# Kernel optimization log

Measured on AMD Instinct MI355X. Metric: run time of the kernel, lower is better.

Reference implementation:

```python
import jax, jax.numpy as jnp
import numpy as np
import math

B, S, KV, D, H = 4, 512, 4096, 1024, 16
HD = D // H  # head_dim = 64


def setup_inputs() -> dict:
    key = jax.random.key(0)
    ks = jax.random.split(key, 12)
    scale = 0.02
    return {
        "x": jax.random.normal(ks[0], (B, S, D), dtype=jnp.float32),
        "xa": jax.random.normal(ks[1], (B, KV, D), dtype=jnp.float32),
        "Wq": jax.random.normal(ks[2], (D, D), dtype=jnp.float32) * scale,
        "bq": jax.random.normal(ks[3], (D,), dtype=jnp.float32) * scale,
        "Wk": jax.random.normal(ks[4], (D, D), dtype=jnp.float32) * scale,  # key has no bias
        "Wv": jax.random.normal(ks[5], (D, D), dtype=jnp.float32) * scale,
        "bv": jax.random.normal(ks[6], (D,), dtype=jnp.float32) * scale,
        "Wo": jax.random.normal(ks[7], (D, D), dtype=jnp.float32) * scale,
        "bo": jax.random.normal(ks[8], (D,), dtype=jnp.float32) * scale,
        "cache_k": jnp.zeros((B, H, KV, HD), dtype=jnp.float32),
        "cache_v": jnp.zeros((B, H, KV, HD), dtype=jnp.float32),
    }


def reference(x, xa, Wq, bq, Wk, Wv, bv, Wo, bo, cache_k, cache_v):
    bsz, seq_len, _ = x.shape
    kv_len = xa.shape[1]
    # projections (torch nn.Linear convention: y = x @ W^T + b)
    q = (x @ Wq.T + bq).reshape(bsz, seq_len, H, HD).transpose(0, 2, 1, 3)   # [B,H,S,HD]
    k = (xa @ Wk.T).reshape(bsz, kv_len, H, HD).transpose(0, 2, 1, 3)        # [B,H,KV,HD]
    v = (xa @ Wv.T + bv).reshape(bsz, kv_len, H, HD).transpose(0, 2, 1, 3)   # [B,H,KV,HD]
    # prefill path: scatter k/v into positions [0, kv_len) of the cache
    updated_k = cache_k.at[:, :, :kv_len, :].set(k)
    updated_v = cache_v.at[:, :, :kv_len, :].set(v)
    # attention over full cache, fp32 softmax as in the original
    scores = jnp.einsum('bhqd,bhkd->bhqk', q, updated_k) / math.sqrt(HD)
    probs = jax.nn.softmax(scores.astype(jnp.float32), axis=-1).astype(q.dtype)
    attn = jnp.einsum('bhqk,bhkd->bhqd', probs, updated_v)                   # [B,H,S,HD]
    attn = attn.transpose(0, 2, 1, 3).reshape(bsz, seq_len, H * HD)
    out = attn @ Wo.T + bo
    return out, updated_k, updated_v
```

## Files before the change

kernel.cpp:

```cpp
#include <hip/hip_runtime.h>
#include <hip/hip_bf16.h>

using u16 = unsigned short;
typedef __bf16 bf16x8 __attribute__((ext_vector_type(8)));
typedef float f32x4 __attribute__((ext_vector_type(4)));

#define SB 4
#define SS 512
#define SKV 4096
#define SD 1024
#define SH 16
#define SHD 64
#define NSPLIT 4
#define NROWS 32768
#define QSCALE 0.18033688011112042f
#define DEFER_THR 6.0f

__device__ inline u16 f2bf(float f){
  __hip_bfloat16 h = __float2bfloat16(f);
  return __builtin_bit_cast(u16, h);
}
__device__ inline float bf2f(u16 u){
  return __builtin_bit_cast(float, (unsigned)u << 16);
}

__device__ inline bf16x8 ld_frag_g(const u16* p){
  uint4 v = *reinterpret_cast<const uint4*>(p);
  return __builtin_bit_cast(bf16x8, v);
}

__device__ inline bf16x8 ld_frag_lds(const char* base, int ob){
  uint4 v = *reinterpret_cast<const uint4*>(base + ob);
  return __builtin_bit_cast(bf16x8, v);
}

__device__ inline unsigned pack_bf_trunc(float a, float b){
  return __builtin_amdgcn_perm(__builtin_bit_cast(unsigned, b),
                               __builtin_bit_cast(unsigned, a), 0x07060302u);
}

__device__ inline uint4 ld_cvt8(const float* p){
  float4 f0 = *reinterpret_cast<const float4*>(p);
  float4 f1 = *reinterpret_cast<const float4*>(p + 4);
  ushort4 a, b;
  a.x = f2bf(f0.x); a.y = f2bf(f0.y); a.z = f2bf(f0.z); a.w = f2bf(f0.w);
  b.x = f2bf(f1.x); b.y = f2bf(f1.y); b.z = f2bf(f1.z); b.w = f2bf(f1.w);
  uint4 r;
  r.x = (unsigned)a.x | ((unsigned)a.y << 16);
  r.y = (unsigned)a.z | ((unsigned)a.w << 16);
  r.z = (unsigned)b.x | ((unsigned)b.y << 16);
  r.w = (unsigned)b.z | ((unsigned)b.w << 16);
  return r;
}

__global__ __launch_bounds__(256) void cast_kernel(const float* __restrict__ src,
                                                   u16* __restrict__ dst, int n4){
  int i = blockIdx.x * 256 + threadIdx.x;
  if (i < n4){
    float4 f = reinterpret_cast<const float4*>(src)[i];
    ushort4 u;
    u.x = f2bf(f.x); u.y = f2bf(f.y); u.z = f2bf(f.z); u.w = f2bf(f.w);
    reinterpret_cast<ushort4*>(dst)[i] = u;
  }
}

__global__ __launch_bounds__(256) void cast_w4(const float* __restrict__ s0,
                                               const float* __restrict__ s1,
                                               const float* __restrict__ s2,
                                               const float* __restrict__ s3,
                                               u16* __restrict__ dst){
  int which = blockIdx.x >> 10;
  int j = (blockIdx.x & 1023) * 256 + threadIdx.x;
  const float* s = which == 0 ? s0 : which == 1 ? s1 : which == 2 ? s2 : s3;
  float4 f = reinterpret_cast<const float4*>(s)[j];
  ushort4 u;
  u.x = f2bf(f.x); u.y = f2bf(f.y); u.z = f2bf(f.z); u.w = f2bf(f.w);
  reinterpret_cast<ushort4*>(dst + (long)which * 1048576L)[j] = u;
}

enum { MODE_Q = 0, MODE_K = 1, MODE_V = 2, MODE_OUT = 3 };

template<int MODE>
__global__ __launch_bounds__(256) void gemm_bt(const u16* __restrict__ A,
                                               const u16* __restrict__ W,
                                               const float* __restrict__ bias,
                                               float* __restrict__ outF,
                                               u16* __restrict__ outB)
{
  __shared__ u16 As[2][128*64];
  __shared__ u16 Bs[2][128*64];
  const int tid  = threadIdx.x;
  const int lane = tid & 63;
  const int wm   = ((tid >> 6) >> 1) * 64;
  const int wn   = ((tid >> 6) & 1) * 64;
  const long rowBase = (long)blockIdx.x * 128;
  const long colBase = (long)blockIdx.y * 128;

  f32x4 acc[4][4];
#pragma unroll
  for (int i = 0; i < 4; i++)
#pragma unroll
    for (int j = 0; j < 4; j++)
      acc[i][j] = (f32x4){0.f, 0.f, 0.f, 0.f};

  uint4 va[4], vw[4];
#pragma unroll
  for (int i = 0; i < 4; i++){
    int u = tid + i * 256;
    int r = u >> 3, c = u & 7;
    va[i] = *reinterpret_cast<const uint4*>(A + (rowBase + r) * 1024 + c * 8);
    vw[i] = *reinterpret_cast<const uint4*>(W + (colBase + r) * 1024 + c * 8);
  }
#pragma unroll
  for (int i = 0; i < 4; i++){
    int u = tid + i * 256;
    int r = u >> 3, c = u & 7;
    int ob = (r * 128 + c * 16) ^ ((r & 7) << 4);
    *reinterpret_cast<uint4*>(reinterpret_cast<char*>(As[0]) + ob) = va[i];
    *reinterpret_cast<uint4*>(reinterpret_cast<char*>(Bs[0]) + ob) = vw[i];
  }
  __syncthreads();

  int cur = 0;
  for (int kt = 0; kt < 16; ++kt){
    uint4 va2[4], vw2[4];
    if (kt < 15){
#pragma unroll
      for (int i = 0; i < 4; i++){
        int u = tid + i * 256;
        int r = u >> 3, c = u & 7;
        va2[i] = *reinterpret_cast<const uint4*>(A + (rowBase + r) * 1024 + (kt + 1) * 64 + c * 8);
        vw2[i] = *reinterpret_cast<const uint4*>(W + (colBase + r) * 1024 + (kt + 1) * 64 + c * 8);
      }
    }
    const char* ach = reinterpret_cast<const char*>(As[cur]);
    const char* bch = reinterpret_cast<const char*>(Bs[cur]);
#pragma unroll
    for (int kk = 0; kk < 2; kk++){
      bf16x8 af[4], bfr[4];
#pragma unroll
      for (int mi = 0; mi < 4; mi++){
        int row = wm + mi * 16 + (lane & 15);
        int ob = (row * 128 + kk * 64 + (lane >> 4) * 16) ^ ((row & 7) << 4);
        af[mi] = ld_frag_lds(ach, ob);
      }
#pragma unroll
      for (int ni = 0; ni < 4; ni++){
        int row = wn + ni * 16 + (lane & 15);
        int ob = (row * 128 + kk * 64 + (lane >> 4) * 16) ^ ((row & 7) << 4);
        bfr[ni] = ld_frag_lds(bch, ob);
      }
#pragma unroll
      for (int mi = 0; mi < 4; mi++)
#pragma unroll
        for (int ni = 0; ni < 4; ni++)
          acc[mi][ni] = __builtin_amdgcn_mfma_f32_16x16x32_bf16(af[mi], bfr[ni], acc[mi][ni], 0, 0, 0);
    }
    if (kt < 15){
#pragma unroll
      for (int i = 0; i < 4; i++){
        int u = tid + i * 256;
        int r = u >> 3, c = u & 7;
        int ob = (r * 128 + c * 16) ^ ((r & 7) << 4);
        *reinterpret_cast<uint4*>(reinterpret_cast<char*>(As[cur ^ 1]) + ob) = va2[i];
        *reinterpret_cast<uint4*>(reinterpret_cast<char*>(Bs[cur ^ 1]) + ob) = vw2[i];
      }
      __syncthreads();
    }
    cur ^= 1;
  }

#pragma unroll
  for (int mi = 0; mi < 4; mi++){
#pragma unroll
    for (int ni = 0; ni < 4; ni++){
      long gn = colBase + wn + ni * 16 + (lane & 15);
      float bb = bias[gn];
#pragma unroll
      for (int r = 0; r < 4; r++){
        long gm = rowBase + wm + mi * 16 + ((lane >> 4) << 2) + r;
        float val = acc[mi][ni][r] + bb;
        if (MODE == MODE_OUT){
          outF[gm * 1024 + gn] = val;
        } else {
          long b = gm >> 9, s = gm & 511;
          long h = gn >> 6, hd = gn & 63;
          outB[((b * SH + h) * SS + s) * SHD + hd] = f2bf(val * QSCALE);
        }
      }
    }
  }
}

__global__ __launch_bounds__(256) void gemm_kv(const float* __restrict__ Axa,
                                               const u16* __restrict__ Wkb,
                                               const u16* __restrict__ Wvb,
                                               const float* __restrict__ bv,
                                               float* __restrict__ outK,
                                               u16* __restrict__ outKb,
                                               float* __restrict__ outV,
                                               u16* __restrict__ outVTb)
{
  __shared__ u16 As[2][128*64];
  __shared__ u16 Bs[2][128*64];
  const int tid  = threadIdx.x;
  const int lane = tid & 63;
  const int wm   = ((tid >> 6) >> 1) * 64;
  const int wn   = ((tid >> 6) & 1) * 64;
  const int lin  = blockIdx.x;
  const int xcd  = lin & 7;
  const int role = (lin >> 3) & 1;
  const int j    = lin >> 4;
  const long rowBase = (long)(xcd * 16 + (j >> 3)) * 128;
  const long colBase = (long)(j & 7) * 128;
  const u16* W = role ? Wvb : Wkb;

  f32x4 acc[4][4];
#pragma unroll
  for (int i = 0; i < 4; i++)
#pragma unroll
    for (int jj = 0; jj < 4; jj++)
      acc[i][jj] = (f32x4){0.f, 0.f, 0.f, 0.f};

  uint4 va[4], vw[4];
#pragma unroll
  for (int i = 0; i < 4; i++){
    int u = tid + i * 256;
    int r = u >> 3, c = u & 7;
    va[i] = ld_cvt8(Axa + (rowBase + r) * 1024 + c * 8);
    vw[i] = *reinterpret_cast<const uint4*>(W + (colBase + r) * 1024 + c * 8);
  }
#pragma unroll
  for (int i = 0; i < 4; i++){
    int u = tid + i * 256;
    int r = u >> 3, c = u & 7;
    int ob = (r * 128 + c * 16) ^ ((r & 7) << 4);
    *reinterpret_cast<uint4*>(reinterpret_cast<char*>(As[0]) + ob) = va[i];
    *reinterpret_cast<uint4*>(reinterpret_cast<char*>(Bs[0]) + ob) = vw[i];
  }
  __syncthreads();

  int cur = 0;
  for (int kt = 0; kt < 16; ++kt){
    uint4 va2[4], vw2[4];
    if (kt < 15){
#pragma unroll
      for (int i = 0; i < 4; i++){
        int u = tid + i * 256;
        int r = u >> 3, c = u & 7;
        va2[i] = ld_cvt8(Axa + (rowBase + r) * 1024 + (kt + 1) * 64 + c * 8);
        vw2[i] = *reinterpret_cast<const uint4*>(W + (colBase + r) * 1024 + (kt + 1) * 64 + c * 8);
      }
    }
    const char* ach = reinterpret_cast<const char*>(As[cur]);
    const char* bch = reinterpret_cast<const char*>(Bs[cur]);
#pragma unroll
    for (int kk = 0; kk < 2; kk++){
      bf16x8 af[4], bfr[4];
#pragma unroll
      for (int mi = 0; mi < 4; mi++){
        int row = wm + mi * 16 + (lane & 15);
        int ob = (row * 128 + kk * 64 + (lane >> 4) * 16) ^ ((row & 7) << 4);
        af[mi] = ld_frag_lds(ach, ob);
      }
#pragma unroll
      for (int ni = 0; ni < 4; ni++){
        int row = wn + ni * 16 + (lane & 15);
        int ob = (row * 128 + kk * 64 + (lane >> 4) * 16) ^ ((row & 7) << 4);
        bfr[ni] = ld_frag_lds(bch, ob);
      }
#pragma unroll
      for (int mi = 0; mi < 4; mi++)
#pragma unroll
        for (int ni = 0; ni < 4; ni++)
          acc[mi][ni] = __builtin_amdgcn_mfma_f32_16x16x32_bf16(af[mi], bfr[ni], acc[mi][ni], 0, 0, 0);
    }
    if (kt < 15){
#pragma unroll
      for (int i = 0; i < 4; i++){
        int u = tid + i * 256;
        int r = u >> 3, c = u & 7;
        int ob = (r * 128 + c * 16) ^ ((r & 7) << 4);
        *reinterpret_cast<uint4*>(reinterpret_cast<char*>(As[cur ^ 1]) + ob) = va2[i];
        *reinterpret_cast<uint4*>(reinterpret_cast<char*>(Bs[cur ^ 1]) + ob) = vw2[i];
      }
      __syncthreads();
    }
    cur ^= 1;
  }

#pragma unroll
  for (int mi = 0; mi < 4; mi++){
#pragma unroll
    for (int ni = 0; ni < 4; ni++){
      long gn = colBase + wn + ni * 16 + (lane & 15);
      long h = gn >> 6, hd = gn & 63;
      if (role){
        float bb = bv[gn];
        long gmBase = rowBase + wm + mi * 16 + ((lane >> 4) << 2);
        long b = gmBase >> 12, kv = gmBase & 4095;
        long fidx = ((b * SH + h) * SKV + kv) * SHD + hd;
        ushort4 pk;
        float v0 = acc[mi][ni][0] + bb; outV[fidx          ] = v0; pk.x = f2bf(v0);
        float v1 = acc[mi][ni][1] + bb; outV[fidx +     SHD] = v1; pk.y = f2bf(v1);
        float v2 = acc[mi][ni][2] + bb; outV[fidx + 2 * SHD] = v2; pk.z = f2bf(v2);
        float v3 = acc[mi][ni][3] + bb; outV[fidx + 3 * SHD] = v3; pk.w = f2bf(v3);
        *reinterpret_cast<ushort4*>(outVTb + ((b * SH + h) * SHD + hd) * SKV + kv) = pk;
      } else {
#pragma unroll
        for (int r = 0; r < 4; r++){
          long gm = rowBase + wm + mi * 16 + ((lane >> 4) << 2) + r;
          long b = gm >> 12, kv = gm & 4095;
          long idx = ((b * SH + h) * SKV + kv) * SHD + hd;
          float val = acc[mi][ni][r];
          outK[idx] = val;
          outKb[idx] = f2bf(val);
        }
      }
    }
  }
}

__global__ __launch_bounds__(512) void attn_partial(const u16* __restrict__ qb,
                                                    const u16* __restrict__ kb,
                                                    const u16* __restrict__ vTb,
                                                    u16* __restrict__ opartB,
                                                    float* __restrict__ ml){
  __shared__ u16 Klds[2][64 * 64];
  __shared__ u16 Vlds[2][64 * 64];
  __shared__ u16 PT[8][16 * 72];
  const int tid  = threadIdx.x;
  const int lane = tid & 63;
  const int wid  = tid >> 6;
  const int c    = lane & 15;
  const int hi   = lane >> 4;
  const long bh  = blockIdx.x;
  const int  qt  = blockIdx.y;
  const int  split = blockIdx.z;

  const u16* qp = qb + (bh * SS + qt * 128 + wid * 16 + c) * SHD + hi * 8;
  const bf16x8 bq0 = ld_frag_g(qp);
  const bf16x8 bq1 = ld_frag_g(qp + 32);

  f32x4 acc[4];
#pragma unroll
  for (int i = 0; i < 4; i++) acc[i] = (f32x4){0.f, 0.f, 0.f, 0.f};
  float mrun = -INFINITY;
  f32x4 lrunv = (f32x4){0.f, 0.f, 0.f, 0.f};

  const u16* kbase = kb  + bh * SKV * SHD;
  const u16* vbase = vTb + bh * SHD * SKV;
  u16* pt = &PT[wid][0];
  const int sr  = tid >> 3;
  const int scc = tid & 7;
  const int sob = (sr * 128 + scc * 16) ^ ((sr & 7) << 4);
  const int t0 = split * 16;

  {
    uint4 kv4 = *reinterpret_cast<const uint4*>(kbase + (t0 * 64 + sr) * SHD + scc * 8);
    uint4 vv4 = *reinterpret_cast<const uint4*>(vbase + (long)sr * SKV + t0 * 64 + scc * 8);
    *reinterpret_cast<uint4*>(reinterpret_cast<char*>(Klds[0]) + sob) = kv4;
    *reinterpret_cast<uint4*>(reinterpret_cast<char*>(Vlds[0]) + sob) = vv4;
  }
  __syncthreads();

  int cur = 0;
  for (int kt = t0; kt < t0 + 16; ++kt){
    const bool hn = kt + 1 < t0 + 16;
    uint4 kn, vn;
    if (hn){
      kn = *reinterpret_cast<const uint4*>(kbase + ((kt + 1) * 64 + sr) * SHD + scc * 8);
      vn = *reinterpret_cast<const uint4*>(vbase + (long)sr * SKV + (kt + 1) * 64 + scc * 8);
    }
    const char* kch = reinterpret_cast<const char*>(Klds[cur]);
    const char* vch = reinterpret_cast<const char*>(Vlds[cur]);

    f32x4 sT[4];
#pragma unroll
    for (int ni = 0; ni < 4; ni++){
      int krow = ni * 16 + c;
      int swz = (krow & 7) << 4;
      int a0 = (krow * 128 + hi * 16) ^ swz;
      int a1 = (krow * 128 + 64 + hi * 16) ^ swz;
      f32x4 z = (f32x4){0.f, 0.f, 0.f, 0.f};
      sT[ni] = __builtin_amdgcn_mfma_f32_16x16x32_bf16(ld_frag_lds(kch, a0), bq0, z, 0, 0, 0);
      sT[ni] = __builtin_amdgcn_mfma_f32_16x16x32_bf16(ld_frag_lds(kch, a1), bq1, sT[ni], 0, 0, 0);
    }
    f32x4 mv = __builtin_elementwise_max(__builtin_elementwise_max(sT[0], sT[1]),
                                         __builtin_elementwise_max(sT[2], sT[3]));
    float t = fmaxf(fmaxf(mv[0], mv[1]), fmaxf(mv[2], mv[3]));
    if (!__all(t <= mrun + DEFER_THR)){
      float tr = fmaxf(t, __shfl_xor(t, 16));
      tr = fmaxf(tr, __shfl_xor(tr, 32));
      float mn = fmaxf(mrun, tr);
      float al = exp2f(mrun - mn);
      lrunv *= al;
#pragma unroll
      for (int ni = 0; ni < 4; ni++) acc[ni] *= al;
      mrun = mn;
    }
#pragma unroll
    for (int ni = 0; ni < 4; ni++){
      f32x4 p;
      p[0] = exp2f(sT[ni][0] - mrun); p[1] = exp2f(sT[ni][1] - mrun);
      p[2] = exp2f(sT[ni][2] - mrun); p[3] = exp2f(sT[ni][3] - mrun);
      lrunv += p;
      unsigned lo = pack_bf_trunc(p[0], p[1]);
      unsigned hp = pack_bf_trunc(p[2], p[3]);
      uint2 w; w.x = lo; w.y = hp;
      *reinterpret_cast<uint2*>(pt + c * 72 + ni * 16 + hi * 4) = w;
    }
#pragma unroll
    for (int m = 0; m < 2; m++){
      bf16x8 pfrag = __builtin_bit_cast(bf16x8,
          *reinterpret_cast<const uint4*>(pt + c * 72 + m * 32 + hi * 8));
#pragma unroll
      for (int ni = 0; ni < 4; ni++){
        int vrow = ni * 16 + c;
        int av = (vrow * 128 + m * 64 + hi * 16) ^ ((vrow & 7) << 4);
        acc[ni] = __builtin_amdgcn_mfma_f32_16x16x32_bf16(ld_frag_lds(vch, av), pfrag, acc[ni], 0, 0, 0);
      }
    }
    if (hn){
      *reinterpret_cast<uint4*>(reinterpret_cast<char*>(Klds[cur ^ 1]) + sob) = kn;
      *reinterpret_cast<uint4*>(reinterpret_cast<char*>(Vlds[cur ^ 1]) + sob) = vn;
      __syncthreads();
    }
    cur ^= 1;
  }

  float l = (lrunv[0] + lrunv[1]) + (lrunv[2] + lrunv[3]);
  l += __shfl_xor(l, 16);
  l += __shfl_xor(l, 32);
  const long row = bh * SS + (long)qt * 128 + wid * 16 + c;
  u16* ob = opartB + ((long)split * NROWS + row) * SHD;
#pragma unroll
  for (int ni = 0; ni < 4; ni++){
    ushort4 pk;
    pk.x = f2bf(acc[ni][0]); pk.y = f2bf(acc[ni][1]);
    pk.z = f2bf(acc[ni][2]); pk.w = f2bf(acc[ni][3]);
    *reinterpret_cast<ushort4*>(ob + ni * 16 + hi * 4) = pk;
  }
  if (hi == 0){
    ml[(long)split * NROWS + row] = mrun;
    ml[(long)NSPLIT * NROWS + (long)split * NROWS + row] = l;
  }
}

__global__ __launch_bounds__(256) void attn_combine(const u16* __restrict__ opartB,
                                                    const float* __restrict__ ml,
                                                    u16* __restrict__ attnb){
  long idx4 = (long)blockIdx.x * 256 + threadIdx.x;
  long row = idx4 >> 4;
  int  c   = (int)(idx4 & 15);
  float m0 = ml[row], m1 = ml[NROWS + row], m2 = ml[2L*NROWS + row], m3 = ml[3L*NROWS + row];
  float M = fmaxf(fmaxf(m0, m1), fmaxf(m2, m3));
  float w0 = exp2f(m0 - M), w1 = exp2f(m1 - M), w2 = exp2f(m2 - M), w3 = exp2f(m3 - M);
  const float* lb = ml + (long)NSPLIT * NROWS;
  float L = w0*lb[row] + w1*lb[NROWS+row] + w2*lb[2L*NROWS+row] + w3*lb[3L*NROWS+row];
  float inv = 1.f / L;
  const ushort4* op = reinterpret_cast<const ushort4*>(opartB);
  ushort4 v0 = op[(0L*NROWS + row) * 16 + c];
  ushort4 v1 = op[(1L*NROWS + row) * 16 + c];
  ushort4 v2 = op[(2L*NROWS + row) * 16 + c];
  ushort4 v3 = op[(3L*NROWS + row) * 16 + c];
  float4 val;
  val.x = (w0*bf2f(v0.x) + w1*bf2f(v1.x) + w2*bf2f(v2.x) + w3*bf2f(v3.x)) * inv;
  val.y = (w0*bf2f(v0.y) + w1*bf2f(v1.y) + w2*bf2f(v2.y) + w3*bf2f(v3.y)) * inv;
  val.z = (w0*bf2f(v0.z) + w1*bf2f(v1.z) + w2*bf2f(v2.z) + w3*bf2f(v3.z)) * inv;
  val.w = (w0*bf2f(v0.w) + w1*bf2f(v1.w) + w2*bf2f(v2.w) + w3*bf2f(v3.w)) * inv;
  long bh = row >> 9, s = row & 511;
  long b = bh >> 4, h = bh & 15;
  ushort4 u;
  u.x = f2bf(val.x); u.y = f2bf(val.y); u.z = f2bf(val.z); u.w = f2bf(val.w);
  reinterpret_cast<ushort4*>(attnb)[((b * SS + s) * SD + h * SHD) / 4 + c] = u;
}

extern "C" void kernel_launch(void* const* d_in, const int* in_sizes, int n_in,
                              void* d_out, int out_size, void* d_ws, size_t ws_size,
                              hipStream_t stream)
{
  const float* x  = (const float*)d_in[0];
  const float* xa = (const float*)d_in[1];
  const float* Wq = (const float*)d_in[2];
  const float* bq = (const float*)d_in[3];
  const float* Wk = (const float*)d_in[4];
  const float* Wv = (const float*)d_in[5];
  const float* bv = (const float*)d_in[6];
  const float* Wo = (const float*)d_in[7];
  const float* bo = (const float*)d_in[8];

  float* outO = (float*)d_out;
  float* outK = outO + (long)SB * SS * SD;
  float* outV = outK + (long)SB * SH * SKV * SHD;

  u16* ws   = (u16*)d_ws;
  u16* xb   = ws;
  u16* xab  = xb   + 2097152L;
  u16* Wqb  = xab  + 16777216L;
  u16* Wkb  = Wqb  + 1048576L;
  u16* Wvb  = Wkb  + 1048576L;
  u16* Wob  = Wvb  + 1048576L;
  u16* qbuf = Wob  + 1048576L;
  u16* kbuf = qbuf + 2097152L;
  u16* vTbuf= kbuf + 16777216L;
  u16* mlb  = vTbuf+ 16777216L;

  u16*   attnb  = xb;
  u16*   opartB = xab;
  float* ml     = (float*)mlb;

  cast_kernel<<<2048, 256, 0, stream>>>(x,  xb,  524288);
  cast_w4    <<<4096, 256, 0, stream>>>(Wq, Wk, Wv, Wo, Wqb);

  gemm_bt<MODE_Q>   <<<dim3(16, 8), 256, 0, stream>>>(xb,  Wqb, bq, nullptr, qbuf);
  gemm_kv           <<<2048,        256, 0, stream>>>(xa, Wkb, Wvb, bv,
                                                      outK, kbuf, outV, vTbuf);
  attn_partial      <<<dim3(64, 4, NSPLIT), 512, 0, stream>>>(qbuf, kbuf, vTbuf, opartB, ml);
  attn_combine      <<<2048, 256, 0, stream>>>(opartB, ml, attnb);
  gemm_bt<MODE_OUT> <<<dim3(16, 8), 256, 0, stream>>>(attnb, Wob, bo, outO, nullptr);
}
```

Measured before the change: 295.3 us.

## Merge cast kernels and fuse Q/K/V projections into a single launch

Folds the x, xa and weight casts into one cast_all kernel, which now also pre-casts xa to bf16. The K/V GEMM therefore loads bf16 instead of converting fp32 in its load path. The Q projection (128 blocks) is merged with the K and V projections into one proj_all launch, so the small Q GEMM no longer leaves most of the GPU idle on its own and there are fewer launches. In exchange, xa makes an extra fp32 read and bf16 write pass through memory. K and V blocks for the same row tile are also no longer interleaved in launch order, which may reduce L2 reuse of xa tiles.

```diff
diff --git a/kernel.cpp b/kernel.cpp
--- a/kernel.cpp
+++ b/kernel.cpp
@@ -39,53 +39,195 @@
                                __builtin_bit_cast(unsigned, a), 0x07060302u);
 }
 
-__device__ inline uint4 ld_cvt8(const float* p){
-  float4 f0 = *reinterpret_cast<const float4*>(p);
-  float4 f1 = *reinterpret_cast<const float4*>(p + 4);
-  ushort4 a, b;
-  a.x = f2bf(f0.x); a.y = f2bf(f0.y); a.z = f2bf(f0.z); a.w = f2bf(f0.w);
-  b.x = f2bf(f1.x); b.y = f2bf(f1.y); b.z = f2bf(f1.z); b.w = f2bf(f1.w);
-  uint4 r;
-  r.x = (unsigned)a.x | ((unsigned)a.y << 16);
-  r.y = (unsigned)a.z | ((unsigned)a.w << 16);
-  r.z = (unsigned)b.x | ((unsigned)b.y << 16);
-  r.w = (unsigned)b.z | ((unsigned)b.w << 16);
-  return r;
-}
-
-__global__ __launch_bounds__(256) void cast_kernel(const float* __restrict__ src,
-                                                   u16* __restrict__ dst, int n4){
-  int i = blockIdx.x * 256 + threadIdx.x;
-  if (i < n4){
-    float4 f = reinterpret_cast<const float4*>(src)[i];
-    ushort4 u;
-    u.x = f2bf(f.x); u.y = f2bf(f.y); u.z = f2bf(f.z); u.w = f2bf(f.w);
-    reinterpret_cast<ushort4*>(dst)[i] = u;
-  }
-}
-
-__global__ __launch_bounds__(256) void cast_w4(const float* __restrict__ s0,
-                                               const float* __restrict__ s1,
-                                               const float* __restrict__ s2,
-                                               const float* __restrict__ s3,
-                                               u16* __restrict__ dst){
-  int which = blockIdx.x >> 10;
-  int j = (blockIdx.x & 1023) * 256 + threadIdx.x;
-  const float* s = which == 0 ? s0 : which == 1 ? s1 : which == 2 ? s2 : s3;
+__global__ __launch_bounds__(256) void cast_all(const float* __restrict__ x,
+                                                const float* __restrict__ xa,
+                                                const float* __restrict__ Wq,
+                                                const float* __restrict__ Wk,
+                                                const float* __restrict__ Wv,
+                                                const float* __restrict__ Wo,
+                                                u16* __restrict__ xb,
+                                                u16* __restrict__ xab,
+                                                u16* __restrict__ Wqb){
+  int bid = blockIdx.x;
+  const float* s; u16* d; long j;
+  if (bid < 2048){
+    s = x;  d = xb;  j = (long)bid * 256 + threadIdx.x;
+  } else if (bid < 18432){
+    s = xa; d = xab; j = (long)(bid - 2048) * 256 + threadIdx.x;
+  } else {
+    int wb = bid - 18432;
+    int which = wb >> 10;
+    s = which == 0 ? Wq : which == 1 ? Wk : which == 2 ? Wv : Wo;
+    d = Wqb + (long)which * 1048576L;
+    j = (long)(wb & 1023) * 256 + threadIdx.x;
+  }
   float4 f = reinterpret_cast<const float4*>(s)[j];
   ushort4 u;
   u.x = f2bf(f.x); u.y = f2bf(f.y); u.z = f2bf(f.z); u.w = f2bf(f.w);
-  reinterpret_cast<ushort4*>(dst + (long)which * 1048576L)[j] = u;
+  reinterpret_cast<ushort4*>(d)[j] = u;
 }
 
 enum { MODE_Q = 0, MODE_K = 1, MODE_V = 2, MODE_OUT = 3 };
 
-template<int MODE>
-__global__ __launch_bounds__(256) void gemm_bt(const u16* __restrict__ A,
-                                               const u16* __restrict__ W,
-                                               const float* __restrict__ bias,
-                                               float* __restrict__ outF,
-                                               u16* __restrict__ outB)
+__global__ __launch_bounds__(256) void proj_all(const u16* __restrict__ xb,
+                                                const u16* __restrict__ xab,
+                                                const u16* __restrict__ Wqb,
+                                                const u16* __restrict__ Wkb,
+                                                const u16* __restrict__ Wvb,
+                                                const float* __restrict__ bq,
+                                                const float* __restrict__ bv,
+                                                u16* __restrict__ qbuf,
+                                                float* __restrict__ outK,
+                                                u16* __restrict__ kbuf,
+                                                float* __restrict__ outV,
+                                                u16* __restrict__ vTbuf)
+{
+  __shared__ u16 As[2][128*64];
+  __shared__ u16 Bs[2][128*64];
+  const int tid  = threadIdx.x;
+  const int lane = tid & 63;
+  const int wm   = ((tid >> 6) >> 1) * 64;
+  const int wn   = ((tid >> 6) & 1) * 64;
+
+  int mode;
+  const u16 *A, *W;
+  long rowBase, colBase;
+  {
+    int bid = blockIdx.x;
+    if (bid < 128){
+      mode = MODE_Q; A = xb; W = Wqb;
+      rowBase = (long)(bid >> 3) * 128;
+      colBase = (long)(bid & 7) * 128;
+    } else {
+      int lin = bid - 128;
+      if (lin < 1024){ mode = MODE_K; W = Wkb; }
+      else           { mode = MODE_V; W = Wvb; lin -= 1024; }
+      A = xab;
+      int xcd = lin & 7, j = lin >> 3;
+      rowBase = (long)(xcd * 16 + (j >> 3)) * 128;
+      colBase = (long)(j & 7) * 128;
+    }
+  }
+
+  f32x4 acc[4][4];
+#pragma unroll
+  for (int i = 0; i < 4; i++)
+#pragma unroll
+    for (int j = 0; j < 4; j++)
+      acc[i][j] = (f32x4){0.f, 0.f, 0.f, 0.f};
+
+  uint4 va[4], vw[4];
+#pragma unroll
+  for (int i = 0; i < 4; i++){
+    int u = tid + i * 256;
+    int r = u >> 3, c = u & 7;
+    va[i] = *reinterpret_cast<const uint4*>(A + (rowBase + r) * 1024 + c * 8);
+    vw[i] = *reinterpret_cast<const uint4*>(W + (colBase + r) * 1024 + c * 8);
+  }
+#pragma unroll
+  for (int i = 0; i < 4; i++){
+    int u = tid + i * 256;
+    int r = u >> 3, c = u & 7;
+    int ob = (r * 128 + c * 16) ^ ((r & 7) << 4);
+    *reinterpret_cast<uint4*>(reinterpret_cast<char*>(As[0]) + ob) = va[i];
+    *reinterpret_cast<uint4*>(reinterpret_cast<char*>(Bs[0]) + ob) = vw[i];
+  }
+  __syncthreads();
+
+  int cur = 0;
+  for (int kt = 0; kt < 16; ++kt){
+    uint4 va2[4], vw2[4];
+    if (kt < 15){
+#pragma unroll
+      for (int i = 0; i < 4; i++){
+        int u = tid + i * 256;
+        int r = u >> 3, c = u & 7;
+        va2[i] = *reinterpret_cast<const uint4*>(A + (rowBase + r) * 1024 + (kt + 1) * 64 + c * 8);
+        vw2[i] = *reinterpret_cast<const uint4*>(W + (colBase + r) * 1024 + (kt + 1) * 64 + c * 8);
+      }
+    }
+    const char* ach = reinterpret_cast<const char*>(As[cur]);
+    const char* bch = reinterpret_cast<const char*>(Bs[cur]);
+#pragma unroll
+    for (int kk = 0; kk < 2; kk++){
+      bf16x8 af[4], bfr[4];
+#pragma unroll
+      for (int mi = 0; mi < 4; mi++){
+        int row = wm + mi * 16 + (lane & 15);
+        int ob = (row * 128 + kk * 64 + (lane >> 4) * 16) ^ ((row & 7) << 4);
+        af[mi] = ld_frag_lds(ach, ob);
+      }
+#pragma unroll
+      for (int ni = 0; ni < 4; ni++){
+        int row = wn + ni * 16 + (lane & 15);
+        int ob = (row * 128 + kk * 64 + (lane >> 4) * 16) ^ ((row & 7) << 4);
+        bfr[ni] = ld_frag_lds(bch, ob);
+      }
+#pragma unroll
+      for (int mi = 0; mi < 4; mi++)
+#pragma unroll
+        for (int ni = 0; ni < 4; ni++)
+          acc[mi][ni] = __builtin_amdgcn_mfma_f32_16x16x32_bf16(af[mi], bfr[ni], acc[mi][ni], 0, 0, 0);
+    }
+    if (kt < 15){
+#pragma unroll
+      for (int i = 0; i < 4; i++){
+        int u = tid + i * 256;
+        int r = u >> 3, c = u & 7;
+        int ob = (r * 128 + c * 16) ^ ((r & 7) << 4);
+        *reinterpret_cast<uint4*>(reinterpret_cast<char*>(As[cur ^ 1]) + ob) = va2[i];
+        *reinterpret_cast<uint4*>(reinterpret_cast<char*>(Bs[cur ^ 1]) + ob) = vw2[i];
+      }
+      __syncthreads();
+    }
+    cur ^= 1;
+  }
+
+#pragma unroll
+  for (int mi = 0; mi < 4; mi++){
+#pragma unroll
+    for (int ni = 0; ni < 4; ni++){
+      long gn = colBase + wn + ni * 16 + (lane & 15);
+      long h = gn >> 6, hd = gn & 63;
+      if (mode == MODE_Q){
+        float bb = bq[gn];
+#pragma unroll
+        for (int r = 0; r < 4; r++){
+          long gm = rowBase + wm + mi * 16 + ((lane >> 4) << 2) + r;
+          long b = gm >> 9, s = gm & 511;
+          qbuf[((b * SH + h) * SS + s) * SHD + hd] =
+              f2bf((acc[mi][ni][r] + bb) * QSCALE);
+        }
+      } else if (mode == MODE_K){
+#pragma unroll
+        for (int r = 0; r < 4; r++){
+          long gm = rowBase + wm + mi * 16 + ((lane >> 4) << 2) + r;
+          long b = gm >> 12, kv = gm & 4095;
+          long idx = ((b * SH + h) * SKV + kv) * SHD + hd;
+          float val = acc[mi][ni][r];
+          outK[idx] = val;
+          kbuf[idx] = f2bf(val);
+        }
+      } else {
+        float bb = bv[gn];
+        long gmBase = rowBase + wm + mi * 16 + ((lane >> 4) << 2);
+        long b = gmBase >> 12, kv = gmBase & 4095;
+        long fidx = ((b * SH + h) * SKV + kv) * SHD + hd;
+        ushort4 pk;
+        float v0 = acc[mi][ni][0] + bb; outV[fidx          ] = v0; pk.x = f2bf(v0);
+        float v1 = acc[mi][ni][1] + bb; outV[fidx +     SHD] = v1; pk.y = f2bf(v1);
+        float v2 = acc[mi][ni][2] + bb; outV[fidx + 2 * SHD] = v2; pk.z = f2bf(v2);
+        float v3 = acc[mi][ni][3] + bb; outV[fidx + 3 * SHD] = v3; pk.w = f2bf(v3);
+        *reinterpret_cast<ushort4*>(vTbuf + ((b * SH + h) * SHD + hd) * SKV + kv) = pk;
+      }
+    }
+  }
+}
+
+__global__ __launch_bounds__(256) void gemm_out(const u16* __restrict__ A,
+                                                const u16* __restrict__ W,
+                                                const float* __restrict__ bias,
+                                                float* __restrict__ outF)
 {
   __shared__ u16 As[2][128*64];
   __shared__ u16 Bs[2][128*64];
@@ -179,143 +321,7 @@
 #pragma unroll
       for (int r = 0; r < 4; r++){
         long gm = rowBase + wm + mi * 16 + ((lane >> 4) << 2) + r;
-        float val = acc[mi][ni][r] + bb;
-        if (MODE == MODE_OUT){
-          outF[gm * 1024 + gn] = val;
-        } else {
-          long b = gm >> 9, s = gm & 511;
-          long h = gn >> 6, hd = gn & 63;
-          outB[((b * SH + h) * SS + s) * SHD + hd] = f2bf(val * QSCALE);
-        }
-      }
-    }
-  }
-}
-
-__global__ __launch_bounds__(256) void gemm_kv(const float* __restrict__ Axa,
-                                               const u16* __restrict__ Wkb,
-                                               const u16* __restrict__ Wvb,
-                                               const float* __restrict__ bv,
-                                               float* __restrict__ outK,
-                                               u16* __restrict__ outKb,
-                                               float* __restrict__ outV,
-                                               u16* __restrict__ outVTb)
-{
-  __shared__ u16 As[2][128*64];
-  __shared__ u16 Bs[2][128*64];
-  const int tid  = threadIdx.x;
-  const int lane = tid & 63;
-  const int wm   = ((tid >> 6) >> 1) * 64;
-  const int wn   = ((tid >> 6) & 1) * 64;
-  const int lin  = blockIdx.x;
-  const int xcd  = lin & 7;
-  const int role = (lin >> 3) & 1;
-  const int j    = lin >> 4;
-  const long rowBase = (long)(xcd * 16 + (j >> 3)) * 128;
-  const long colBase = (long)(j & 7) * 128;
-  const u16* W = role ? Wvb : Wkb;
-
-  f32x4 acc[4][4];
-#pragma unroll
-  for (int i = 0; i < 4; i++)
-#pragma unroll
-    for (int jj = 0; jj < 4; jj++)
-      acc[i][jj] = (f32x4){0.f, 0.f, 0.f, 0.f};
-
-  uint4 va[4], vw[4];
-#pragma unroll
-  for (int i = 0; i < 4; i++){
-    int u = tid + i * 256;
-    int r = u >> 3, c = u & 7;
-    va[i] = ld_cvt8(Axa + (rowBase + r) * 1024 + c * 8);
-    vw[i] = *reinterpret_cast<const uint4*>(W + (colBase + r) * 1024 + c * 8);
-  }
-#pragma unroll
-  for (int i = 0; i < 4; i++){
-    int u = tid + i * 256;
-    int r = u >> 3, c = u & 7;
-    int ob = (r * 128 + c * 16) ^ ((r & 7) << 4);
-    *reinterpret_cast<uint4*>(reinterpret_cast<char*>(As[0]) + ob) = va[i];
-    *reinterpret_cast<uint4*>(reinterpret_cast<char*>(Bs[0]) + ob) = vw[i];
-  }
-  __syncthreads();
-
-  int cur = 0;
-  for (int kt = 0; kt < 16; ++kt){
-    uint4 va2[4], vw2[4];
-    if (kt < 15){
-#pragma unroll
-      for (int i = 0; i < 4; i++){
-        int u = tid + i * 256;
-        int r = u >> 3, c = u & 7;
-        va2[i] = ld_cvt8(Axa + (rowBase + r) * 1024 + (kt + 1) * 64 + c * 8);
-        vw2[i] = *reinterpret_cast<const uint4*>(W + (colBase + r) * 1024 + (kt + 1) * 64 + c * 8);
-      }
-    }
-    const char* ach = reinterpret_cast<const char*>(As[cur]);
-    const char* bch = reinterpret_cast<const char*>(Bs[cur]);
-#pragma unroll
-    for (int kk = 0; kk < 2; kk++){
-      bf16x8 af[4], bfr[4];
-#pragma unroll
-      for (int mi = 0; mi < 4; mi++){
-        int row = wm + mi * 16 + (lane & 15);
-        int ob = (row * 128 + kk * 64 + (lane >> 4) * 16) ^ ((row & 7) << 4);
-        af[mi] = ld_frag_lds(ach, ob);
-      }
-#pragma unroll
-      for (int ni = 0; ni < 4; ni++){
-        int row = wn + ni * 16 + (lane & 15);
-        int ob = (row * 128 + kk * 64 + (lane >> 4) * 16) ^ ((row & 7) << 4);
-        bfr[ni] = ld_frag_lds(bch, ob);
-      }
-#pragma unroll
-      for (int mi = 0; mi < 4; mi++)
-#pragma unroll
-        for (int ni = 0; ni < 4; ni++)
-          acc[mi][ni] = __builtin_amdgcn_mfma_f32_16x16x32_bf16(af[mi], bfr[ni], acc[mi][ni], 0, 0, 0);
-    }
-    if (kt < 15){
-#pragma unroll
-      for (int i = 0; i < 4; i++){
-        int u = tid + i * 256;
-        int r = u >> 3, c = u & 7;
-        int ob = (r * 128 + c * 16) ^ ((r & 7) << 4);
-        *reinterpret_cast<uint4*>(reinterpret_cast<char*>(As[cur ^ 1]) + ob) = va2[i];
-        *reinterpret_cast<uint4*>(reinterpret_cast<char*>(Bs[cur ^ 1]) + ob) = vw2[i];
-      }
-      __syncthreads();
-    }
-    cur ^= 1;
-  }
-
-#pragma unroll
-  for (int mi = 0; mi < 4; mi++){
-#pragma unroll
-    for (int ni = 0; ni < 4; ni++){
-      long gn = colBase + wn + ni * 16 + (lane & 15);
-      long h = gn >> 6, hd = gn & 63;
-      if (role){
-        float bb = bv[gn];
-        long gmBase = rowBase + wm + mi * 16 + ((lane >> 4) << 2);
-        long b = gmBase >> 12, kv = gmBase & 4095;
-        long fidx = ((b * SH + h) * SKV + kv) * SHD + hd;
-        ushort4 pk;
-        float v0 = acc[mi][ni][0] + bb; outV[fidx          ] = v0; pk.x = f2bf(v0);
-        float v1 = acc[mi][ni][1] + bb; outV[fidx +     SHD] = v1; pk.y = f2bf(v1);
-        float v2 = acc[mi][ni][2] + bb; outV[fidx + 2 * SHD] = v2; pk.z = f2bf(v2);
-        float v3 = acc[mi][ni][3] + bb; outV[fidx + 3 * SHD] = v3; pk.w = f2bf(v3);
-        *reinterpret_cast<ushort4*>(outVTb + ((b * SH + h) * SHD + hd) * SKV + kv) = pk;
-      } else {
-#pragma unroll
-        for (int r = 0; r < 4; r++){
-          long gm = rowBase + wm + mi * 16 + ((lane >> 4) << 2) + r;
-          long b = gm >> 12, kv = gm & 4095;
-          long idx = ((b * SH + h) * SKV + kv) * SHD + hd;
-          float val = acc[mi][ni][r];
-          outK[idx] = val;
-          outKb[idx] = f2bf(val);
-        }
+        outF[gm * 1024 + gn] = acc[mi][ni][r] + bb;
       }
     }
   }
@@ -510,13 +516,11 @@
   u16*   opartB = xab;
   float* ml     = (float*)mlb;
 
-  cast_kernel<<<2048, 256, 0, stream>>>(x,  xb,  524288);
-  cast_w4    <<<4096, 256, 0, stream>>>(Wq, Wk, Wv, Wo, Wqb);
-
-  gemm_bt<MODE_Q>   <<<dim3(16, 8), 256, 0, stream>>>(xb,  Wqb, bq, nullptr, qbuf);
-  gemm_kv           <<<2048,        256, 0, stream>>>(xa, Wkb, Wvb, bv,
-                                                      outK, kbuf, outV, vTbuf);
-  attn_partial      <<<dim3(64, 4, NSPLIT), 512, 0, stream>>>(qbuf, kbuf, vTbuf, opartB, ml);
-  attn_combine      <<<2048, 256, 0, stream>>>(opartB, ml, attnb);
-  gemm_bt<MODE_OUT> <<<dim3(16, 8), 256, 0, stream>>>(attnb, Wob, bo, outO, nullptr);
-}
+  cast_all<<<22528, 256, 0, stream>>>(x, xa, Wq, Wk, Wv, Wo, xb, xab, Wqb);
+
+  proj_all<<<2176, 256, 0, stream>>>(xb, xab, Wqb, Wkb, Wvb, bq, bv,
+                                     qbuf, outK, kbuf, outV, vTbuf);
+  attn_partial<<<dim3(64, 4, NSPLIT), 512, 0, stream>>>(qbuf, kbuf, vTbuf, opartB, ml);
+  attn_combine<<<2048, 256, 0, stream>>>(opartB, ml, attnb);
+  gemm_out    <<<dim3(16, 8), 256, 0, stream>>>(attnb, Wob, bo, outO);
+}
```

Result: faster. 243.0 us (median of 2 runs) (-17.7%).
